# Kernel tuning notes

Measured on AMD Instinct MI355X. Metric: run time of the kernel, lower is better.

Reference implementation:

```python
import jax, jax.numpy as jnp
import numpy as np

# ---- module hyper-params (from init_kwargs) ----
NTYPES = 2
SEL = (46, 92)          # neighbors selected per type, ordered by type
NNEI = sum(SEL)         # 138
RCUT = 6.0
RCUT_SMTH = 0.5
NEURON = (24, 48, 96)   # embedding net widths, input dim = 1 (the s(r) value)
AXIS = 8                # axis_neuron

# ---- problem size ----
NF = 2
NATOMS = 4096
BOX = 12.0              # small box so random pairs fall inside rcut (correctness baseline)


def setup_inputs() -> dict:
    key = jax.random.key(0)
    ks = jax.random.split(key, 10)
    coord = jax.random.uniform(ks[0], (NF, NATOMS, 3), dtype=jnp.float32) * BOX
    atype = jax.random.randint(ks[1], (NF, NATOMS), 0, NTYPES, dtype=jnp.int32)
    nlist = jax.random.randint(ks[2], (NF, NATOMS, NNEI), 0, NATOMS, dtype=jnp.int32)
    davg = jnp.zeros((NTYPES, NNEI, 4), jnp.float32)
    dstd = jnp.ones((NTYPES, NNEI, 4), jnp.float32)

    def w(k, shape):
        return (jax.random.normal(k, shape, jnp.float32) / np.float32(np.sqrt(shape[-2])))

    W1 = w(ks[3], (NTYPES, 1, NEURON[0]))
    b1 = jax.random.normal(ks[4], (NTYPES, NEURON[0]), jnp.float32) * 0.1
    W2 = w(ks[5], (NTYPES, NEURON[0], NEURON[1]))
    b2 = jax.random.normal(ks[6], (NTYPES, NEURON[1]), jnp.float32) * 0.1
    W3 = w(ks[7], (NTYPES, NEURON[1], NEURON[2]))
    b3 = jax.random.normal(ks[8], (NTYPES, NEURON[2]), jnp.float32) * 0.1
    return dict(coord=coord, davg=davg, dstd=dstd,
                W1=W1, b1=b1, W2=W2, b2=b2, W3=W3, b3=b3,
                atype=atype, nlist=nlist)


def _embed(x, W1, b1, W2, b2, W3, b3):
    # DeepMD embedding net with resnet doubling skips: 1 -> 24 -> 48 -> 96
    h1 = jnp.tanh(x @ W1 + b1)
    h2 = jnp.tanh(h1 @ W2 + b2)
    x2 = jnp.concatenate([h1, h1], axis=-1) + h2          # 24 -> 48 (double)
    h3 = jnp.tanh(x2 @ W3 + b3)
    return jnp.concatenate([x2, x2], axis=-1) + h3        # 48 -> 96 (double)


def reference(coord, davg, dstd, W1, b1, W2, b2, W3, b3, atype, nlist):
    # ---- prod_env_mat_a: build smoothed env matrix from neighbor gathers ----
    nc = jax.vmap(lambda c, nl: c[nl])(coord, nlist)       # [NF, NA, NNEI, 3]
    rij = nc - coord[:, :, None, :]
    rsq = jnp.sum(rij * rij, axis=-1)
    r = jnp.sqrt(jnp.maximum(rsq, 1e-12))
    uu = (r - RCUT_SMTH) / (RCUT - RCUT_SMTH)
    vv = uu * uu * uu * (-6.0 * uu * uu + 15.0 * uu - 10.0) + 1.0
    sw = jnp.where(r < RCUT_SMTH, 1.0, jnp.where(r < RCUT, vv, 0.0))
    s = sw / r                                             # s(r) = sw(r)/r
    env = jnp.concatenate([s[..., None], (s / r)[..., None] * rij], axis=-1)  # [NF,NA,NNEI,4]
    d = (env - davg[atype]) / dstd[atype]                  # normalize per atom type

    # ---- per-neighbor-type embedding MLP on the s-channel ----
    Gs, start = [], 0
    for t in range(NTYPES):
        seg = d[:, :, start:start + SEL[t], 0:1]
        Gs.append(_embed(seg, W1[t], b1[t], W2[t], b2[t], W3[t], b3[t]))
        start += SEL[t]
    G = jnp.concatenate(Gs, axis=2)                        # [NF, NA, NNEI, M]

    # ---- descriptor contraction: D = (R^T G / nnei)^T (R^T G / nnei)[:, :axis] ----
    gr = jnp.einsum('fnia,fnim->fnam', d, G) / np.float32(NNEI)  # [NF,NA,4,M]
    D = jnp.einsum('fnam,fnak->fnmk', gr, gr[..., :AXIS])        # [NF,NA,M,AXIS]
    return D.reshape(NF, NATOMS, NEURON[-1] * AXIS)
```

## Files before the change

### kernel.cpp

```cpp
#include <hip/hip_runtime.h>

#define NFRAME 2
#define NATOMS 4096
#define NNEI 138
#define SEL0 46
#define N1 24
#define N2 48
#define N3 96

#define NTAB 4096
#define UMIN (-17.0f)
#define DUF (37.0f / 4095.0f)
#define INVDU (4095.0f / 37.0f)
#define XMINF 7.62939453125e-6f
#define ROWB 192
#define ZOFF (2 * NTAB * ROWB)

#define FIB 0
#define DFB 640
#define GRB 1920
#define SMEM_BYTES 3456

using short8 = __attribute__((ext_vector_type(8))) short;
using f32x4  = __attribute__((ext_vector_type(4))) float;

__device__ __forceinline__ float fexp2(float x) {
#if __has_builtin(__builtin_amdgcn_exp2f)
    return __builtin_amdgcn_exp2f(x);
#else
    return exp2f(x);
#endif
}
__device__ __forceinline__ float frcp(float x) {
#if __has_builtin(__builtin_amdgcn_rcpf)
    return __builtin_amdgcn_rcpf(x);
#else
    return 1.0f / x;
#endif
}
__device__ __forceinline__ float fast_tanh(float x) {
    float e = fexp2(x * 2.8853900817779268f);
    return 1.0f - 2.0f * frcp(e + 1.0f);
}
__device__ __forceinline__ unsigned int f2bf(float f) {
    unsigned int u = __float_as_uint(f);
    return (u + 0x7fffu + ((u >> 16) & 1u)) >> 16;
}
__device__ __forceinline__ unsigned int cvt_pk_bf16(float a, float b) {
    unsigned int r;
    asm("v_cvt_pk_bf16_f32 %0, %1, %2" : "=v"(r) : "v"(a), "v"(b));
    return r;
}

__global__ __launch_bounds__(256) void prep_table(
    const float* __restrict__ W1, const float* __restrict__ b1,
    const float* __restrict__ W2, const float* __restrict__ b2,
    const float* __restrict__ W3, const float* __restrict__ b3,
    unsigned short* __restrict__ tab)
{
    __shared__ float h1s[4][32];
    __shared__ float x2s[4][48];

    if (blockIdx.x == 0 && threadIdx.x < 96)
        tab[(size_t)2 * NTAB * 96 + threadIdx.x] = 0;

    const int esub = threadIdx.x >> 6;
    const int lane = threadIdx.x & 63;
    const int t  = blockIdx.x * 4 + esub;
    const int ty = t >> 12;
    const int e  = t & (NTAB - 1);
    const float x = fexp2(UMIN + (float)e * DUF);

    if (lane < N1)
        h1s[esub][lane] = fast_tanh(fmaf(x, W1[ty * N1 + lane], b1[ty * N1 + lane]));
    __syncthreads();

    if (lane < N2) {
        float acc = b2[ty * N2 + lane];
        #pragma unroll
        for (int k = 0; k < N1; ++k)
            acc = fmaf(h1s[esub][k], W2[(ty * N1 + k) * N2 + lane], acc);
        const int jm = (lane < N1) ? lane : (lane - N1);
        x2s[esub][lane] = h1s[esub][jm] + fast_tanh(acc);
    }
    __syncthreads();

    unsigned short* orow = tab + (size_t)t * N3;
    {
        float acc0 = b3[ty * N3 + lane];
        float acc1 = (lane < 32) ? b3[ty * N3 + 64 + lane] : 0.0f;
        #pragma unroll 8
        for (int k = 0; k < N2; ++k) {
            const float xk = x2s[esub][k];
            acc0 = fmaf(xk, W3[(ty * N2 + k) * N3 + lane], acc0);
            if (lane < 32)
                acc1 = fmaf(xk, W3[(ty * N2 + k) * N3 + 64 + lane], acc1);
        }
        const int jm0 = (lane < N2) ? lane : (lane - N2);
        orow[lane] = (unsigned short)f2bf(x2s[esub][jm0] + fast_tanh(acc0));
        if (lane < 32)
            orow[64 + lane] = (unsigned short)f2bf(x2s[esub][16 + lane] + fast_tanh(acc1));
    }
}

__global__ __launch_bounds__(192) __attribute__((amdgpu_waves_per_eu(4)))
void descrpt_sea_kernel(
    const float* __restrict__ coord,
    const float* __restrict__ davg,
    const float* __restrict__ dstd,
    const int* __restrict__ atype, const int* __restrict__ nlist,
    const unsigned short* __restrict__ tab,
    float* __restrict__ out)
{
    __shared__ float smemf[SMEM_BYTES / 4];
    unsigned char* smemb = reinterpret_cast<unsigned char*>(smemf);
    const unsigned char* tabb = reinterpret_cast<const unsigned char*>(tab);

    const int bid  = blockIdx.x;
    const int f    = bid >> 12;
    const int tid  = threadIdx.x;
    const int wid  = tid >> 6;
    const int lane = tid & 63;
    const int cl   = lane & 15;
    const int grp  = lane >> 4;

    int i;
    bool active;
    if (wid == 0)      { i = lane;             active = (lane < SEL0); }
    else if (wid == 1) { i = SEL0 + lane;      active = true; }
    else               { i = SEL0 + 64 + lane; active = (i < NNEI); }
    const int tseg = __builtin_amdgcn_readfirstlane((wid == 0) ? 0 : 1);
    const int prow = (i < SEL0) ? i : (i + 2);

    const float cx = coord[bid * 3 + 0];
    const float cy = coord[bid * 3 + 1];
    const float cz = coord[bid * 3 + 2];
    const int at = atype[bid];

    if (tid < 88) {
        const int t = tid >> 2;
        const int row = (t < 2) ? (46 + t) : (138 + t);
        const int a = tid & 3;
        const int byte = DFB + ((row >> 5) << 8) + ((((row >> 3) & 3) * 4 + a) << 4)
                       + ((row & 7) << 1);
        *reinterpret_cast<unsigned short*>(smemb + byte) = 0;
    }
    if (tid < 22) {
        const int row = (tid < 2) ? (46 + tid) : (138 + tid);
        *reinterpret_cast<unsigned int*>(smemb + FIB + row * 4) = (unsigned int)ZOFF;
    }

    if (active) {
        const int nl = nlist[bid * NNEI + i];
        const float* nc = coord + ((size_t)f * NATOMS + (size_t)nl) * 3;
        float dx = nc[0] - cx, dy = nc[1] - cy, dz = nc[2] - cz;
        float rsq = dx * dx + dy * dy + dz * dz;
        float r = sqrtf(fmaxf(rsq, 1e-12f));
        float uu = (r - 0.5f) * (1.0f / 5.5f);
        float vv = uu * uu * uu * (uu * (-6.0f * uu + 15.0f) - 10.0f) + 1.0f;
        float sw = (r < 0.5f) ? 1.0f : ((r < 6.0f) ? vv : 0.0f);
        float rinv = frcp(r);
        float s = sw * rinv;
        float sor = s * rinv;
        const float* avg  = davg + ((size_t)at * NNEI + i) * 4;
        const float* stdp = dstd + ((size_t)at * NNEI + i) * 4;
        const float d0 = (s        - avg[0]) * frcp(stdp[0]);
        const float d1 = (sor * dx - avg[1]) * frcp(stdp[1]);
        const float d2 = (sor * dy - avg[2]) * frcp(stdp[2]);
        const float d3 = (sor * dz - avg[3]) * frcp(stdp[3]);

        const unsigned int u01 = cvt_pk_bf16(d0, d1);
        const unsigned int u23 = cvt_pk_bf16(d2, d3);
        const int dbase = DFB + ((prow >> 5) << 8) + ((((prow >> 3) & 3) * 4) << 4)
                        + ((prow & 7) << 1);
        *reinterpret_cast<unsigned short*>(smemb + dbase +  0) = (unsigned short)u01;
        *reinterpret_cast<unsigned short*>(smemb + dbase + 16) = (unsigned short)(u01 >> 16);
        *reinterpret_cast<unsigned short*>(smemb + dbase + 32) = (unsigned short)u23;
        *reinterpret_cast<unsigned short*>(smemb + dbase + 48) = (unsigned short)(u23 >> 16);

        const float xin = fmaxf(d0, XMINF);
        float fi = (log2f(xin) - UMIN) * INVDU;
        fi = fminf(fmaxf(fi, 0.0f), (float)(NTAB - 1));
        int i0 = (int)(fi + 0.5f);
        i0 = (i0 < NTAB - 1) ? i0 : (NTAB - 1);
        const unsigned int off = (unsigned int)((tseg * NTAB + i0) * ROWB);
        *reinterpret_cast<unsigned int*>(smemb + FIB + prow * 4) = off;
    }

    __syncthreads();

    const short8 zero8 = (short8){0,0,0,0,0,0,0,0};
    short8 af[5];
    #pragma unroll
    for (int ks = 0; ks < 5; ++ks) {
        short8 v = zero8;
        if (cl < 4)
            v = *reinterpret_cast<const short8*>(smemb + DFB + (ks << 8) + ((grp * 4 + cl) << 4));
        af[ks] = v;
    }

    const int c2g0 = ((wid * 2 + 0) * 16 + cl) * 2;
    const int c2g1 = ((wid * 2 + 1) * 16 + cl) * 2;
    f32x4 racc0 = (f32x4){0.f, 0.f, 0.f, 0.f};
    f32x4 racc1 = (f32x4){0.f, 0.f, 0.f, 0.f};
    #pragma unroll
    for (int ks = 0; ks < 5; ++ks) {
        unsigned int off[8];
        #pragma unroll
        for (int j = 0; j < 8; ++j)
            off[j] = *reinterpret_cast<const unsigned int*>(
                smemb + FIB + (ks * 32 + grp * 8 + j) * 4);
        unsigned int g0[8], g1[8];
        #pragma unroll
        for (int j = 0; j < 8; ++j) {
            g0[j] = *reinterpret_cast<const unsigned short*>(tabb + off[j] + c2g0);
            g1[j] = *reinterpret_cast<const unsigned short*>(tabb + off[j] + c2g1);
        }
        uint4 q0, q1;
        q0.x = g0[0] | (g0[1] << 16); q0.y = g0[2] | (g0[3] << 16);
        q0.z = g0[4] | (g0[5] << 16); q0.w = g0[6] | (g0[7] << 16);
        q1.x = g1[0] | (g1[1] << 16); q1.y = g1[2] | (g1[3] << 16);
        q1.z = g1[4] | (g1[5] << 16); q1.w = g1[6] | (g1[7] << 16);
        racc0 = __builtin_amdgcn_mfma_f32_16x16x32_bf16(
            af[ks], *reinterpret_cast<const short8*>(&q0), racc0, 0, 0, 0);
        racc1 = __builtin_amdgcn_mfma_f32_16x16x32_bf16(
            af[ks], *reinterpret_cast<const short8*>(&q1), racc1, 0, 0, 0);
    }

    if (grp == 0) {
        const float inv = 1.0f / (float)NNEI;
        #pragma unroll
        for (int q = 0; q < 4; ++q) {
            *reinterpret_cast<float*>(smemb + GRB + (q * 96 + (wid * 2 + 0) * 16 + cl) * 4) =
                racc0[q] * inv;
            *reinterpret_cast<float*>(smemb + GRB + (q * 96 + (wid * 2 + 1) * 16 + cl) * 4) =
                racc1[q] * inv;
        }
    }

    __syncthreads();

    {
        const float* gr = reinterpret_cast<const float*>(smemb + GRB);
        const size_t base = (size_t)bid * 768;
        const int kk = tid & 7;
        float gk[4];
        #pragma unroll
        for (int a = 0; a < 4; ++a) gk[a] = gr[a * 96 + kk];
        #pragma unroll
        for (int rep = 0; rep < 4; ++rep) {
            const int o  = tid + rep * 192;
            const int mm = o >> 3;
            float a0v = 0.0f;
            #pragma unroll
            for (int a = 0; a < 4; ++a)
                a0v = fmaf(gr[a * 96 + mm], gk[a], a0v);
            out[base + o] = a0v;
        }
    }
}

extern "C" void kernel_launch(void* const* d_in, const int* in_sizes, int n_in,
                              void* d_out, int out_size, void* d_ws, size_t ws_size,
                              hipStream_t stream) {
    const float* coord = (const float*)d_in[0];
    const float* davg  = (const float*)d_in[1];
    const float* dstd  = (const float*)d_in[2];
    const float* W1    = (const float*)d_in[3];
    const float* b1    = (const float*)d_in[4];
    const float* W2    = (const float*)d_in[5];
    const float* b2    = (const float*)d_in[6];
    const float* W3    = (const float*)d_in[7];
    const float* b3    = (const float*)d_in[8];
    const int*   atype = (const int*)d_in[9];
    const int*   nlist = (const int*)d_in[10];
    float* out = (float*)d_out;
    unsigned short* tab = (unsigned short*)d_ws;

    prep_table<<<dim3(2 * NTAB / 4), dim3(256), 0, stream>>>(
        W1, b1, W2, b2, W3, b3, tab);
    descrpt_sea_kernel<<<dim3(NFRAME * NATOMS), dim3(192), 0, stream>>>(
        coord, davg, dstd, atype, nlist, tab, out);
}
```

Before: 48.43 us.

## Use single-wave blocks per atom and shuffle-based table prep

The main kernel now runs one 64-lane wave per atom instead of three waves. Each lane loops over up to three neighbors, and the wave computes all six MFMA column tiles itself, so the block barriers become single-wave syncs. The table-prep kernel replaces its shared-memory staging and barriers with wave shuffles. This removes cross-wave synchronization and block overhead, but it lengthens each wave's serial work and raises register use for six accumulators, which may reduce latency hiding for the table gathers.

```diff
diff --git a/kernel.cpp b/kernel.cpp
--- a/kernel.cpp
+++ b/kernel.cpp
@@ -58,9 +58,6 @@
     const float* __restrict__ W3, const float* __restrict__ b3,
     unsigned short* __restrict__ tab)
 {
-    __shared__ float h1s[4][32];
-    __shared__ float x2s[4][48];
-
     if (blockIdx.x == 0 && threadIdx.x < 96)
         tab[(size_t)2 * NTAB * 96 + threadIdx.x] = 0;
 
@@ -71,19 +68,24 @@
     const int e  = t & (NTAB - 1);
     const float x = fexp2(UMIN + (float)e * DUF);
 
+    float h1 = 0.0f;
     if (lane < N1)
-        h1s[esub][lane] = fast_tanh(fmaf(x, W1[ty * N1 + lane], b1[ty * N1 + lane]));
-    __syncthreads();
-
-    if (lane < N2) {
-        float acc = b2[ty * N2 + lane];
-        #pragma unroll
-        for (int k = 0; k < N1; ++k)
-            acc = fmaf(h1s[esub][k], W2[(ty * N1 + k) * N2 + lane], acc);
+        h1 = fast_tanh(fmaf(x, W1[ty * N1 + lane], b1[ty * N1 + lane]));
+
+    float x2 = 0.0f;
+    {
+        float acc = (lane < N2) ? b2[ty * N2 + lane] : 0.0f;
+        #pragma unroll
+        for (int k = 0; k < N1; ++k) {
+            const float hk = __shfl(h1, k, 64);
+            if (lane < N2)
+                acc = fmaf(hk, W2[(ty * N1 + k) * N2 + lane], acc);
+        }
         const int jm = (lane < N1) ? lane : (lane - N1);
-        x2s[esub][lane] = h1s[esub][jm] + fast_tanh(acc);
-    }
-    __syncthreads();
+        const float h1jm = __shfl(h1, jm, 64);
+        if (lane < N2)
+            x2 = h1jm + fast_tanh(acc);
+    }
 
     unsigned short* orow = tab + (size_t)t * N3;
     {
@@ -91,19 +93,21 @@
         float acc1 = (lane < 32) ? b3[ty * N3 + 64 + lane] : 0.0f;
         #pragma unroll 8
         for (int k = 0; k < N2; ++k) {
-            const float xk = x2s[esub][k];
+            const float xk = __shfl(x2, k, 64);
             acc0 = fmaf(xk, W3[(ty * N2 + k) * N3 + lane], acc0);
             if (lane < 32)
                 acc1 = fmaf(xk, W3[(ty * N2 + k) * N3 + 64 + lane], acc1);
         }
         const int jm0 = (lane < N2) ? lane : (lane - N2);
-        orow[lane] = (unsigned short)f2bf(x2s[esub][jm0] + fast_tanh(acc0));
+        const float xj0 = __shfl(x2, jm0, 64);
+        const float xj1 = __shfl(x2, 16 + (lane & 31), 64);
+        orow[lane] = (unsigned short)f2bf(xj0 + fast_tanh(acc0));
         if (lane < 32)
-            orow[64 + lane] = (unsigned short)f2bf(x2s[esub][16 + lane] + fast_tanh(acc1));
-    }
-}
-
-__global__ __launch_bounds__(192) __attribute__((amdgpu_waves_per_eu(4)))
+            orow[64 + lane] = (unsigned short)f2bf(xj1 + fast_tanh(acc1));
+    }
+}
+
+__global__ __launch_bounds__(64)
 void descrpt_sea_kernel(
     const float* __restrict__ coord,
     const float* __restrict__ davg,
@@ -118,73 +122,69 @@
 
     const int bid  = blockIdx.x;
     const int f    = bid >> 12;
-    const int tid  = threadIdx.x;
-    const int wid  = tid >> 6;
-    const int lane = tid & 63;
+    const int lane = threadIdx.x;
     const int cl   = lane & 15;
     const int grp  = lane >> 4;
-
-    int i;
-    bool active;
-    if (wid == 0)      { i = lane;             active = (lane < SEL0); }
-    else if (wid == 1) { i = SEL0 + lane;      active = true; }
-    else               { i = SEL0 + 64 + lane; active = (i < NNEI); }
-    const int tseg = __builtin_amdgcn_readfirstlane((wid == 0) ? 0 : 1);
-    const int prow = (i < SEL0) ? i : (i + 2);
 
     const float cx = coord[bid * 3 + 0];
     const float cy = coord[bid * 3 + 1];
     const float cz = coord[bid * 3 + 2];
     const int at = atype[bid];
 
-    if (tid < 88) {
-        const int t = tid >> 2;
+    for (int z = lane; z < 88; z += 64) {
+        const int t = z >> 2;
         const int row = (t < 2) ? (46 + t) : (138 + t);
-        const int a = tid & 3;
+        const int a = z & 3;
         const int byte = DFB + ((row >> 5) << 8) + ((((row >> 3) & 3) * 4 + a) << 4)
                        + ((row & 7) << 1);
         *reinterpret_cast<unsigned short*>(smemb + byte) = 0;
     }
-    if (tid < 22) {
-        const int row = (tid < 2) ? (46 + tid) : (138 + tid);
+    if (lane < 22) {
+        const int row = (lane < 2) ? (46 + lane) : (138 + lane);
         *reinterpret_cast<unsigned int*>(smemb + FIB + row * 4) = (unsigned int)ZOFF;
     }
 
-    if (active) {
-        const int nl = nlist[bid * NNEI + i];
-        const float* nc = coord + ((size_t)f * NATOMS + (size_t)nl) * 3;
-        float dx = nc[0] - cx, dy = nc[1] - cy, dz = nc[2] - cz;
-        float rsq = dx * dx + dy * dy + dz * dz;
-        float r = sqrtf(fmaxf(rsq, 1e-12f));
-        float uu = (r - 0.5f) * (1.0f / 5.5f);
-        float vv = uu * uu * uu * (uu * (-6.0f * uu + 15.0f) - 10.0f) + 1.0f;
-        float sw = (r < 0.5f) ? 1.0f : ((r < 6.0f) ? vv : 0.0f);
-        float rinv = frcp(r);
-        float s = sw * rinv;
-        float sor = s * rinv;
-        const float* avg  = davg + ((size_t)at * NNEI + i) * 4;
-        const float* stdp = dstd + ((size_t)at * NNEI + i) * 4;
-        const float d0 = (s        - avg[0]) * frcp(stdp[0]);
-        const float d1 = (sor * dx - avg[1]) * frcp(stdp[1]);
-        const float d2 = (sor * dy - avg[2]) * frcp(stdp[2]);
-        const float d3 = (sor * dz - avg[3]) * frcp(stdp[3]);
-
-        const unsigned int u01 = cvt_pk_bf16(d0, d1);
-        const unsigned int u23 = cvt_pk_bf16(d2, d3);
-        const int dbase = DFB + ((prow >> 5) << 8) + ((((prow >> 3) & 3) * 4) << 4)
-                        + ((prow & 7) << 1);
-        *reinterpret_cast<unsigned short*>(smemb + dbase +  0) = (unsigned short)u01;
-        *reinterpret_cast<unsigned short*>(smemb + dbase + 16) = (unsigned short)(u01 >> 16);
-        *reinterpret_cast<unsigned short*>(smemb + dbase + 32) = (unsigned short)u23;
-        *reinterpret_cast<unsigned short*>(smemb + dbase + 48) = (unsigned short)(u23 >> 16);
-
-        const float xin = fmaxf(d0, XMINF);
-        float fi = (log2f(xin) - UMIN) * INVDU;
-        fi = fminf(fmaxf(fi, 0.0f), (float)(NTAB - 1));
-        int i0 = (int)(fi + 0.5f);
-        i0 = (i0 < NTAB - 1) ? i0 : (NTAB - 1);
-        const unsigned int off = (unsigned int)((tseg * NTAB + i0) * ROWB);
-        *reinterpret_cast<unsigned int*>(smemb + FIB + prow * 4) = off;
+    #pragma unroll
+    for (int it = 0; it < 3; ++it) {
+        const int idx = it * 64 + lane;
+        if (idx < NNEI) {
+            const int tseg = (idx < SEL0) ? 0 : 1;
+            const int prow = (idx < SEL0) ? idx : (idx + 2);
+            const int nl = nlist[bid * NNEI + idx];
+            const float* nc = coord + ((size_t)f * NATOMS + (size_t)nl) * 3;
+            float dx = nc[0] - cx, dy = nc[1] - cy, dz = nc[2] - cz;
+            float rsq = dx * dx + dy * dy + dz * dz;
+            float r = sqrtf(fmaxf(rsq, 1e-12f));
+            float uu = (r - 0.5f) * (1.0f / 5.5f);
+            float vv = uu * uu * uu * (uu * (-6.0f * uu + 15.0f) - 10.0f) + 1.0f;
+            float sw = (r < 0.5f) ? 1.0f : ((r < 6.0f) ? vv : 0.0f);
+            float rinv = frcp(r);
+            float s = sw * rinv;
+            float sor = s * rinv;
+            const float* avg  = davg + ((size_t)at * NNEI + idx) * 4;
+            const float* stdp = dstd + ((size_t)at * NNEI + idx) * 4;
+            const float d0 = (s        - avg[0]) * frcp(stdp[0]);
+            const float d1 = (sor * dx - avg[1]) * frcp(stdp[1]);
+            const float d2 = (sor * dy - avg[2]) * frcp(stdp[2]);
+            const float d3 = (sor * dz - avg[3]) * frcp(stdp[3]);
+
+            const unsigned int u01 = cvt_pk_bf16(d0, d1);
+            const unsigned int u23 = cvt_pk_bf16(d2, d3);
+            const int dbase = DFB + ((prow >> 5) << 8) + ((((prow >> 3) & 3) * 4) << 4)
+                            + ((prow & 7) << 1);
+            *reinterpret_cast<unsigned short*>(smemb + dbase +  0) = (unsigned short)u01;
+            *reinterpret_cast<unsigned short*>(smemb + dbase + 16) = (unsigned short)(u01 >> 16);
+            *reinterpret_cast<unsigned short*>(smemb + dbase + 32) = (unsigned short)u23;
+            *reinterpret_cast<unsigned short*>(smemb + dbase + 48) = (unsigned short)(u23 >> 16);
+
+            const float xin = fmaxf(d0, XMINF);
+            float fi = (log2f(xin) - UMIN) * INVDU;
+            fi = fminf(fmaxf(fi, 0.0f), (float)(NTAB - 1));
+            int i0 = (int)(fi + 0.5f);
+            i0 = (i0 < NTAB - 1) ? i0 : (NTAB - 1);
+            *reinterpret_cast<unsigned int*>(smemb + FIB + prow * 4) =
+                (unsigned int)((tseg * NTAB + i0) * ROWB);
+        }
     }
 
     __syncthreads();
@@ -199,10 +199,10 @@
         af[ks] = v;
     }
 
-    const int c2g0 = ((wid * 2 + 0) * 16 + cl) * 2;
-    const int c2g1 = ((wid * 2 + 1) * 16 + cl) * 2;
-    f32x4 racc0 = (f32x4){0.f, 0.f, 0.f, 0.f};
-    f32x4 racc1 = (f32x4){0.f, 0.f, 0.f, 0.f};
+    f32x4 racc[6];
+    #pragma unroll
+    for (int ntg = 0; ntg < 6; ++ntg) racc[ntg] = (f32x4){0.f, 0.f, 0.f, 0.f};
+
     #pragma unroll
     for (int ks = 0; ks < 5; ++ks) {
         unsigned int off[8];
@@ -210,32 +210,29 @@
         for (int j = 0; j < 8; ++j)
             off[j] = *reinterpret_cast<const unsigned int*>(
                 smemb + FIB + (ks * 32 + grp * 8 + j) * 4);
-        unsigned int g0[8], g1[8];
-        #pragma unroll
-        for (int j = 0; j < 8; ++j) {
-            g0[j] = *reinterpret_cast<const unsigned short*>(tabb + off[j] + c2g0);
-            g1[j] = *reinterpret_cast<const unsigned short*>(tabb + off[j] + c2g1);
-        }
-        uint4 q0, q1;
-        q0.x = g0[0] | (g0[1] << 16); q0.y = g0[2] | (g0[3] << 16);
-        q0.z = g0[4] | (g0[5] << 16); q0.w = g0[6] | (g0[7] << 16);
-        q1.x = g1[0] | (g1[1] << 16); q1.y = g1[2] | (g1[3] << 16);
-        q1.z = g1[4] | (g1[5] << 16); q1.w = g1[6] | (g1[7] << 16);
-        racc0 = __builtin_amdgcn_mfma_f32_16x16x32_bf16(
-            af[ks], *reinterpret_cast<const short8*>(&q0), racc0, 0, 0, 0);
-        racc1 = __builtin_amdgcn_mfma_f32_16x16x32_bf16(
-            af[ks], *reinterpret_cast<const short8*>(&q1), racc1, 0, 0, 0);
+        #pragma unroll
+        for (int ntg = 0; ntg < 6; ++ntg) {
+            const int c2 = (ntg * 16 + cl) * 2;
+            unsigned int g[8];
+            #pragma unroll
+            for (int j = 0; j < 8; ++j)
+                g[j] = *reinterpret_cast<const unsigned short*>(tabb + off[j] + c2);
+            uint4 q;
+            q.x = g[0] | (g[1] << 16); q.y = g[2] | (g[3] << 16);
+            q.z = g[4] | (g[5] << 16); q.w = g[6] | (g[7] << 16);
+            racc[ntg] = __builtin_amdgcn_mfma_f32_16x16x32_bf16(
+                af[ks], *reinterpret_cast<const short8*>(&q), racc[ntg], 0, 0, 0);
+        }
     }
 
     if (grp == 0) {
         const float inv = 1.0f / (float)NNEI;
         #pragma unroll
-        for (int q = 0; q < 4; ++q) {
-            *reinterpret_cast<float*>(smemb + GRB + (q * 96 + (wid * 2 + 0) * 16 + cl) * 4) =
-                racc0[q] * inv;
-            *reinterpret_cast<float*>(smemb + GRB + (q * 96 + (wid * 2 + 1) * 16 + cl) * 4) =
-                racc1[q] * inv;
-        }
+        for (int ntg = 0; ntg < 6; ++ntg)
+            #pragma unroll
+            for (int q = 0; q < 4; ++q)
+                *reinterpret_cast<float*>(smemb + GRB + (q * 96 + ntg * 16 + cl) * 4) =
+                    racc[ntg][q] * inv;
     }
 
     __syncthreads();
@@ -243,13 +240,13 @@
     {
         const float* gr = reinterpret_cast<const float*>(smemb + GRB);
         const size_t base = (size_t)bid * 768;
-        const int kk = tid & 7;
+        const int kk = lane & 7;
         float gk[4];
         #pragma unroll
         for (int a = 0; a < 4; ++a) gk[a] = gr[a * 96 + kk];
         #pragma unroll
-        for (int rep = 0; rep < 4; ++rep) {
-            const int o  = tid + rep * 192;
+        for (int rep = 0; rep < 12; ++rep) {
+            const int o  = lane + rep * 64;
             const int mm = o >> 3;
             float a0v = 0.0f;
             #pragma unroll
@@ -279,6 +276,6 @@
 
     prep_table<<<dim3(2 * NTAB / 4), dim3(256), 0, stream>>>(
         W1, b1, W2, b2, W3, b3, tab);
-    descrpt_sea_kernel<<<dim3(NFRAME * NATOMS), dim3(192), 0, stream>>>(
+    descrpt_sea_kernel<<<dim3(NFRAME * NATOMS), dim3(64), 0, stream>>>(
         coord, davg, dstd, atype, nlist, tab, out);
 }
```

Measured after the change: 51.22 us. 1.06x slower.
